# Kernel optimization log

Hardware: AMD Instinct MI355X
Metric: run time of the kernel (lower is better)

Reference implementation:

```python
import jax, jax.numpy as jnp
import numpy as np
from jax.scipy.linalg import solve_triangular

L_SUB = 16          # subarray length (init arg L)
DL = 0.05           # diagonal loading factor


def setup_inputs() -> dict:
    key = jax.random.key(0)
    k0, k1, k2 = jax.random.split(key, 3)
    B, C, NS, NZ, NX = 2, 128, 1024, 256, 128
    rf = jax.random.normal(k0, (B, C, NS), jnp.float32)
    t0 = jnp.zeros((B,), jnp.float32)
    d_tx = jax.random.uniform(k1, (B, NZ, NX), dtype=jnp.float32)
    d_rx = jax.random.uniform(k2, (C, NZ, NX), dtype=jnp.float32)
    fs = jnp.float32((NS - 1) / 2.0)   # keeps sample positions in [0, NS-1]
    f0 = jnp.float32(5.0)              # unused by forward (kept for signature parity)
    c0 = jnp.float32(1.0)
    apod = jnp.ones((C,), jnp.float32) # unused by forward
    return dict(rf=rf, t0=t0, d_tx=d_tx, d_rx=d_rx, fs=fs, f0=f0, c0=c0, apod=apod)


def _aligned_signals(rf, t0, d_tx, d_rx, fs, c0):
    """Bilinear (1-D linear) resample of rf at per-pixel delays.
    Equivalent to torch grid_sample(mode='bilinear', padding_mode='border',
    align_corners=True) where the grid x-coord is samples*2/(NS-1)-1."""
    B, C, NS = rf.shape
    _, NZ, NX = d_tx.shape
    # samples: [B, C, NZ, NX] fractional sample index into rf
    samples = fs * ((d_tx[:, None, :, :] + d_rx[None, :, :, :]) / c0
                    + t0[:, None, None, None])
    pos = jnp.clip(samples, 0.0, NS - 1.0)          # border padding
    i0 = jnp.floor(pos).astype(jnp.int32)
    i1 = jnp.minimum(i0 + 1, NS - 1)
    frac = pos - i0.astype(pos.dtype)
    sig = rf.reshape(B * C, NS)
    i0f = i0.reshape(B * C, NZ * NX)
    i1f = i1.reshape(B * C, NZ * NX)
    v0 = jnp.take_along_axis(sig, i0f, axis=1).reshape(B, C, NZ, NX)
    v1 = jnp.take_along_axis(sig, i1f, axis=1).reshape(B, C, NZ, NX)
    return v0 * (1.0 - frac) + v1 * frac


def reference(rf, t0, d_tx, d_rx, fs, f0, c0, apod):
    B, C, NS = rf.shape
    _, NZ, NX = d_tx.shape
    M = C - L_SUB + 1  # number of subarrays (113)
    aligned = _aligned_signals(rf, t0, d_tx, d_rx, fs, c0)  # [B, C, NZ, NX]
    # per-pixel channel vectors: [P, C], P = B*NZ*NX
    xf = aligned.transpose(0, 2, 3, 1).reshape(-1, C)
    # subarray gather: S[p, m, l] = xf[p, m + l]  -> [P, M, L]
    idx = jnp.arange(M)[:, None] + jnp.arange(L_SUB)[None, :]
    S = xf[:, idx]
    # avg_pool1d(kernel=M, stride=1) over channels == mean over subarray axis
    x = S.mean(axis=1)                                  # [P, L]
    # spatially-smoothed covariance: R = S^T S / M, symmetrized
    R = jnp.einsum('pml,pmk->plk', S, S) / M
    R = 0.5 * (R + R.transpose(0, 2, 1))
    # diagonal loading: R += dl * (trace/L) * I
    delta = jnp.trace(R, axis1=-2, axis2=-1) / L_SUB    # [P]
    R = R + (DL * delta)[:, None, None] * jnp.eye(L_SUB, dtype=R.dtype)
    # Cholesky solve R u = 1
    Lc = jnp.linalg.cholesky(R)
    rhs = jnp.ones((R.shape[0], L_SUB, 1), R.dtype)
    y1 = solve_triangular(Lc, rhs, lower=True)
    u = solve_triangular(Lc, y1, lower=True, trans=1)[..., 0]  # [P, L]
    # MVDR weights (steering a = ones) and beamformed output
    denom = jnp.sum(u, axis=-1, keepdims=True) + 1e-10
    w = u / denom
    y = jnp.sum(w * x, axis=-1)                         # [P]
    return y.reshape(B, NZ, NX)
```

## Files before the change

### kernel.cpp

```cpp
#include <hip/hip_runtime.h>


namespace {

constexpr int kB  = 2;
constexpr int kC  = 128;
constexpr int kNS = 1024;
constexpr int kNZ = 256;
constexpr int kNX = 128;
constexpr int kZX = kNZ * kNX;
constexpr int kTPB = 256;

__device__ __host__ constexpr int tri(int l, int k) {
  return l * 16 - (l * (l - 1)) / 2 + (k - l);
}

template <bool HEAD>
__device__ __forceinline__ void chunk16(
    const float* __restrict__ rfq,
    const float* __restrict__ drxp, int cbase, float kk, float base,
    float (&F)[16], float (&win)[16], float (&head)[16], float& Sall) {
  float dr[16];
#pragma unroll
  for (int r = 0; r < 16; ++r) dr[r] = drxp[(size_t)(cbase + r) * kZX];

  float2 vv[16];
  float fr[16];
#pragma unroll
  for (int r = 0; r < 16; ++r) {
    float pos = fmaf(kk, dr[r], base);
    pos = fminf(fmaxf(pos, 0.0f), 1023.0f);
    int i0 = (int)pos;
    i0 = min(i0, kNS - 2);
    fr[r] = pos - (float)i0;
    __builtin_memcpy(&vv[r], rfq + r * kNS + i0, 8);
  }

#pragma unroll
  for (int r = 0; r < 16; ++r) {
    float v = fmaf(fr[r], vv[r].y - vv[r].x, vv[r].x);
    Sall += v;
    F[0] = fmaf(v, v, F[0]);
    if constexpr (HEAD) {
#pragma unroll
      for (int d = 1; d <= r; ++d) F[d] = fmaf(v, win[r - d], F[d]);
      head[r] = v;
    } else {
#pragma unroll
      for (int d = 1; d < 16; ++d) F[d] = fmaf(v, win[(r - d) & 15], F[d]);
    }
    win[r] = v;
  }
}

__global__ __launch_bounds__(kTPB, 1) void mvb_kernel(
    const float* __restrict__ rf, const float* __restrict__ t0,
    const float* __restrict__ d_tx, const float* __restrict__ d_rx,
    const float* __restrict__ fs_p, const float* __restrict__ c0_p,
    float* __restrict__ out) {
  const int tid = threadIdx.x;
  const int b = blockIdx.x >> 7;
  const int z = ((blockIdx.x & 127) << 1) + (tid >> 7);
  const int x = tid & 127;
  const int pix = (int)((size_t)b * kZX + z * kNX + x);

  const float fs = fs_p[0];
  const float c0 = c0_p[0];
  const float kk = fs / c0;
  const float base = fs * (d_tx[pix] / c0 + t0[b]);

  const float* rfb = rf + (size_t)b * kC * kNS;
  const float* drxp = d_rx + (size_t)z * kNX + x;

  float F[16], win[16], head[16];
  float Sall = 0.0f;
#pragma unroll
  for (int i = 0; i < 16; ++i) F[i] = 0.0f;

  chunk16<true>(rfb, drxp, 0, kk, base, F, win, head, Sall);
#pragma unroll 1
  for (int q = 1; q < 8; ++q)
    chunk16<false>(rfb + (size_t)q * 16 * kNS, drxp, q * 16, kk, base, F, win,
                   head, Sall);

  float Ru[136];
#pragma unroll
  for (int d = 0; d < 16; ++d) {
    float t0s = 0.0f;
#pragma unroll
    for (int i = d + 1; i < 16; ++i) t0s = fmaf(win[i - d], win[i], t0s);
    Ru[tri(0, d)] = F[d] - t0s;
#pragma unroll
    for (int l = 1; l < 16 - d; ++l)
      Ru[tri(l, l + d)] = Ru[tri(l - 1, l - 1 + d)] -
                          head[l - 1] * head[l - 1 + d] +
                          win[l] * win[l + d];
  }

  float tr = 0.0f;
#pragma unroll
  for (int l = 0; l < 16; ++l) tr += Ru[tri(l, l)];
  const float dl = tr * (0.05f / 16.0f);
#pragma unroll
  for (int l = 0; l < 16; ++l) Ru[tri(l, l)] += dl;

  float X[16];
  {
    float s = Sall;
#pragma unroll
    for (int i = 1; i < 16; ++i) s -= win[i];
    X[0] = s;
#pragma unroll
    for (int l = 1; l < 16; ++l) X[l] = X[l - 1] - head[l - 1] + win[l];
  }

  float inv[16];
#pragma unroll
  for (int j = 0; j < 16; ++j) {
    float d = Ru[tri(j, j)];
#pragma unroll
    for (int p = 0; p < j; ++p) d = fmaf(-Ru[tri(p, j)], Ru[tri(p, j)], d);
    inv[j] = rsqrtf(d);
#pragma unroll
    for (int i = j + 1; i < 16; ++i) {
      float s = Ru[tri(j, i)];
#pragma unroll
      for (int p = 0; p < j; ++p) s = fmaf(-Ru[tri(p, i)], Ru[tri(p, j)], s);
      Ru[tri(j, i)] = s * inv[j];
    }
  }

  float yv[16];
#pragma unroll
  for (int i = 0; i < 16; ++i) {
    float s = 1.0f;
#pragma unroll
    for (int j = 0; j < i; ++j) s = fmaf(-Ru[tri(j, i)], yv[j], s);
    yv[i] = s * inv[i];
  }
  float u[16];
#pragma unroll
  for (int i = 15; i >= 0; --i) {
    float s = yv[i];
#pragma unroll
    for (int j = i + 1; j < 16; ++j) s = fmaf(-Ru[tri(i, j)], u[j], s);
    u[i] = s * inv[i];
  }

  float su = 0.0f, dot = 0.0f;
#pragma unroll
  for (int i = 0; i < 16; ++i) {
    su += u[i];
    dot = fmaf(u[i], X[i], dot);
  }
  out[pix] = dot / (113.0f * su + 1e-10f);
}

}

extern "C" void kernel_launch(void* const* d_in, const int* in_sizes, int n_in,
                              void* d_out, int out_size, void* d_ws,
                              size_t ws_size, hipStream_t stream) {
  const float* rf   = (const float*)d_in[0];
  const float* t0   = (const float*)d_in[1];
  const float* d_tx = (const float*)d_in[2];
  const float* d_rx = (const float*)d_in[3];
  const float* fs   = (const float*)d_in[4];
  const float* c0   = (const float*)d_in[6];
  float* out = (float*)d_out;

  hipLaunchKernelGGL(mvb_kernel, dim3(kB * kNZ / 2), dim3(kTPB), 0, stream,
                     rf, t0, d_tx, d_rx, fs, c0, out);
}
```

Measured before the change: 94.92 us.

## Split channel accumulation across two thread halves and merge partial sums through LDS

Each pixel's 128-channel accumulation is now split between two threads, each handling 64 channels. The block covers one z row instead of two, and the grid doubles. The lower half writes its partial correlation lags, window and head to shared memory. The upper half then merges them, adding the cross-boundary products, and runs the Cholesky solve alone. This halves the serial gather chain per thread and doubles the number of waves available to hide memory latency. The cost is shared-memory traffic, a barrier, and half the threads sitting idle during the solve phase.

After: 97.22 us. 1.02x slower.

```diff
diff --git a/kernel.cpp b/kernel.cpp
--- a/kernel.cpp
+++ b/kernel.cpp
@@ -58,30 +58,64 @@
     const float* __restrict__ d_tx, const float* __restrict__ d_rx,
     const float* __restrict__ fs_p, const float* __restrict__ c0_p,
     float* __restrict__ out) {
+  __shared__ float xch[49 * 128];
+
   const int tid = threadIdx.x;
-  const int b = blockIdx.x >> 7;
-  const int z = ((blockIdx.x & 127) << 1) + (tid >> 7);
-  const int x = tid & 127;
-  const int pix = (int)((size_t)b * kZX + z * kNX + x);
+  const int half = tid >> 7;
+  const int px = tid & 127;
+  const int z = blockIdx.x & (kNZ - 1);
+  const int b = blockIdx.x >> 8;
+  const int pix = (int)((size_t)b * kZX + z * kNX + px);
 
   const float fs = fs_p[0];
   const float c0 = c0_p[0];
   const float kk = fs / c0;
   const float base = fs * (d_tx[pix] / c0 + t0[b]);
 
-  const float* rfb = rf + (size_t)b * kC * kNS;
-  const float* drxp = d_rx + (size_t)z * kNX + x;
+  const float* rfh = rf + (size_t)b * kC * kNS + (size_t)half * 64 * kNS;
+  const float* drxp =
+      d_rx + (size_t)half * 64 * kZX + (size_t)z * kNX + px;
 
   float F[16], win[16], head[16];
   float Sall = 0.0f;
 #pragma unroll
   for (int i = 0; i < 16; ++i) F[i] = 0.0f;
 
-  chunk16<true>(rfb, drxp, 0, kk, base, F, win, head, Sall);
+  chunk16<true>(rfh, drxp, 0, kk, base, F, win, head, Sall);
 #pragma unroll 1
-  for (int q = 1; q < 8; ++q)
-    chunk16<false>(rfb + (size_t)q * 16 * kNS, drxp, q * 16, kk, base, F, win,
-                   head, Sall);
+  for (int q = 1; q < 4; ++q)
+    chunk16<false>(rfh + (size_t)q * 16 * kNS, drxp, q * 16, kk, base, F,
+                   win, head, Sall);
+
+  if (half == 0) {
+#pragma unroll
+    for (int i = 0; i < 16; ++i) xch[i * 128 + px] = F[i];
+#pragma unroll
+    for (int i = 0; i < 16; ++i) xch[(16 + i) * 128 + px] = win[i];
+#pragma unroll
+    for (int i = 0; i < 16; ++i) xch[(32 + i) * 128 + px] = head[i];
+    xch[48 * 128 + px] = Sall;
+  }
+  __syncthreads();
+  if (half == 0) return;
+
+  float hlo[16];
+  {
+    float wlo[16];
+#pragma unroll
+    for (int i = 0; i < 16; ++i) wlo[i] = xch[(16 + i) * 128 + px];
+#pragma unroll
+    for (int i = 0; i < 16; ++i) hlo[i] = xch[(32 + i) * 128 + px];
+    Sall += xch[48 * 128 + px];
+    F[0] += xch[0 * 128 + px];
+#pragma unroll
+    for (int d = 1; d < 16; ++d) {
+      float s = xch[d * 128 + px];
+#pragma unroll
+      for (int i = 0; i < d; ++i) s = fmaf(head[i], wlo[16 - d + i], s);
+      F[d] += s;
+    }
+  }
 
   float Ru[136];
 #pragma unroll
@@ -93,7 +127,7 @@
 #pragma unroll
     for (int l = 1; l < 16 - d; ++l)
       Ru[tri(l, l + d)] = Ru[tri(l - 1, l - 1 + d)] -
-                          head[l - 1] * head[l - 1 + d] +
+                          hlo[l - 1] * hlo[l - 1 + d] +
                           win[l] * win[l + d];
   }
 
@@ -111,7 +145,7 @@
     for (int i = 1; i < 16; ++i) s -= win[i];
     X[0] = s;
 #pragma unroll
-    for (int l = 1; l < 16; ++l) X[l] = X[l - 1] - head[l - 1] + win[l];
+    for (int l = 1; l < 16; ++l) X[l] = X[l - 1] - hlo[l - 1] + win[l];
   }
 
   float inv[16];
@@ -169,6 +203,6 @@
   const float* c0   = (const float*)d_in[6];
   float* out = (float*)d_out;
 
-  hipLaunchKernelGGL(mvb_kernel, dim3(kB * kNZ / 2), dim3(kTPB), 0, stream,
+  hipLaunchKernelGGL(mvb_kernel, dim3(kB * kNZ), dim3(kTPB), 0, stream,
                      rf, t0, d_tx, d_rx, fs, c0, out);
 }
```

## Software-pipeline d_rx loads and rf gathers across channel chunks

Applied to the files above, without the earlier changes.

Replaces the serial per-chunk loop (load delays, gather, accumulate) with a fully unrolled three-stage software pipeline. Delays for chunk c+2 and the rf gather for chunk c+1 are issued before the FMA accumulation of chunk c, so memory latency overlaps with compute. This raises register pressure, holding up to three delay buffers and two gather buffers, which at launch_bounds(256,1) may cause spills.

Measured after the change: 108.9 us. 1.15x slower.

```diff
diff --git a/kernel.cpp b/kernel.cpp
--- a/kernel.cpp
+++ b/kernel.cpp
@@ -15,30 +15,36 @@
   return l * 16 - (l * (l - 1)) / 2 + (k - l);
 }
 
-template <bool HEAD>
-__device__ __forceinline__ void chunk16(
-    const float* __restrict__ rfq,
-    const float* __restrict__ drxp, int cbase, float kk, float base,
-    float (&F)[16], float (&win)[16], float (&head)[16], float& Sall) {
-  float dr[16];
-#pragma unroll
-  for (int r = 0; r < 16; ++r) dr[r] = drxp[(size_t)(cbase + r) * kZX];
-
-  float2 vv[16];
-  float fr[16];
+struct Dr16  { float d[16]; };
+struct Gth16 { float2 vv[16]; float fr[16]; };
+
+__device__ __forceinline__ void load_dr(const float* __restrict__ drxp,
+                                        int cbase, Dr16& o) {
+#pragma unroll
+  for (int r = 0; r < 16; ++r) o.d[r] = drxp[(size_t)(cbase + r) * kZX];
+}
+
+__device__ __forceinline__ void gather16(const float* __restrict__ rfq,
+                                         const Dr16& dr, float kk, float base,
+                                         Gth16& o) {
 #pragma unroll
   for (int r = 0; r < 16; ++r) {
-    float pos = fmaf(kk, dr[r], base);
+    float pos = fmaf(kk, dr.d[r], base);
     pos = fminf(fmaxf(pos, 0.0f), 1023.0f);
     int i0 = (int)pos;
     i0 = min(i0, kNS - 2);
-    fr[r] = pos - (float)i0;
-    __builtin_memcpy(&vv[r], rfq + r * kNS + i0, 8);
-  }
-
+    o.fr[r] = pos - (float)i0;
+    __builtin_memcpy(&o.vv[r], rfq + r * kNS + i0, 8);
+  }
+}
+
+template <bool HEAD>
+__device__ __forceinline__ void fmas16(const Gth16& g, float (&F)[16],
+                                       float (&win)[16], float (&head)[16],
+                                       float& Sall) {
 #pragma unroll
   for (int r = 0; r < 16; ++r) {
-    float v = fmaf(fr[r], vv[r].y - vv[r].x, vv[r].x);
+    float v = fmaf(g.fr[r], g.vv[r].y - g.vv[r].x, g.vv[r].x);
     Sall += v;
     F[0] = fmaf(v, v, F[0]);
     if constexpr (HEAD) {
@@ -69,7 +75,7 @@
   const float kk = fs / c0;
   const float base = fs * (d_tx[pix] / c0 + t0[b]);
 
-  const float* rfb = rf + (size_t)b * kC * kNS;
+  const float* rfb = rfb = rf + (size_t)b * kC * kNS;
   const float* drxp = d_rx + (size_t)z * kNX + x;
 
   float F[16], win[16], head[16];
@@ -77,11 +83,37 @@
 #pragma unroll
   for (int i = 0; i < 16; ++i) F[i] = 0.0f;
 
-  chunk16<true>(rfb, drxp, 0, kk, base, F, win, head, Sall);
-#pragma unroll 1
-  for (int q = 1; q < 8; ++q)
-    chunk16<false>(rfb + (size_t)q * 16 * kNS, drxp, q * 16, kk, base, F, win,
-                   head, Sall);
+  Dr16 drA, drB, drC;
+  Gth16 gA, gB;
+
+#define RFQ(c) (rfb + (size_t)(c) * 16 * kNS)
+
+  load_dr(drxp, 0 * 16, drA);
+  load_dr(drxp, 1 * 16, drB);
+  gather16(RFQ(0), drA, kk, base, gA);
+
+  load_dr(drxp, 2 * 16, drC);
+  gather16(RFQ(1), drB, kk, base, gB);
+  fmas16<true>(gA, F, win, head, Sall);
+  load_dr(drxp, 3 * 16, drA);
+  gather16(RFQ(2), drC, kk, base, gA);
+  fmas16<false>(gB, F, win, head, Sall);
+  load_dr(drxp, 4 * 16, drB);
+  gather16(RFQ(3), drA, kk, base, gB);
+  fmas16<false>(gA, F, win, head, Sall);
+  load_dr(drxp, 5 * 16, drC);
+  gather16(RFQ(4), drB, kk, base, gA);
+  fmas16<false>(gB, F, win, head, Sall);
+  load_dr(drxp, 6 * 16, drA);
+  gather16(RFQ(5), drC, kk, base, gB);
+  fmas16<false>(gA, F, win, head, Sall);
+  load_dr(drxp, 7 * 16, drB);
+  gather16(RFQ(6), drA, kk, base, gA);
+  fmas16<false>(gB, F, win, head, Sall);
+  gather16(RFQ(7), drB, kk, base, gB);
+  fmas16<false>(gA, F, win, head, Sall);
+  fmas16<false>(gB, F, win, head, Sall);
+#undef RFQ
 
   float Ru[136];
 #pragma unroll
```
